# Kernel tuning notes

Hardware: AMD Instinct MI355X
Metric: run time of the kernel (lower is better)

## Reference

```python
import jax, jax.numpy as jnp
import numpy as np

D_MODEL = 768
HEAD_SIZE = 64

def setup_inputs() -> dict:
    key = jax.random.key(0)
    ks = jax.random.split(key, 7)
    B, S = 8, 2048
    x = jax.random.normal(ks[0], (B, S, D_MODEL), dtype=jnp.float32)
    s = 1.0 / np.sqrt(D_MODEL)
    Wq = jax.random.uniform(ks[1], (D_MODEL, HEAD_SIZE), jnp.float32, -s, s)
    bq = jnp.zeros((HEAD_SIZE,), jnp.float32)
    Wk = jax.random.uniform(ks[2], (D_MODEL, HEAD_SIZE), jnp.float32, -s, s)
    bk = jnp.zeros((HEAD_SIZE,), jnp.float32)
    Wv = jax.random.uniform(ks[3], (D_MODEL, HEAD_SIZE), jnp.float32, -s, s)
    bv = jnp.zeros((HEAD_SIZE,), jnp.float32)
    return {"x": x, "Wq": Wq, "bq": bq, "Wk": Wk, "bk": bk, "Wv": Wv, "bv": bv}

def reference(x, Wq, bq, Wk, bk, Wv, bv):
    # Single attention head: softmax(Q K^T / sqrt(head_size)) V
    q = jnp.einsum('bsd,dh->bsh', x, Wq) + bq  # [B,S,H]
    k = jnp.einsum('bsd,dh->bsh', x, Wk) + bk
    v = jnp.einsum('bsd,dh->bsh', x, Wv) + bv
    scale = 1.0 / jnp.sqrt(jnp.array(HEAD_SIZE, dtype=x.dtype))
    scores = jnp.einsum('bqh,bkh->bqk', q, k) * scale  # [B,S,S]
    attn = jax.nn.softmax(scores, axis=-1)
    out = jnp.einsum('bqk,bkh->bqh', attn, v)  # [B,S,H]
    return out
```

## Files before the change

kernel.cpp:

```cpp
#include <hip/hip_runtime.h>
#include <math.h>

#define D_MODEL 768
#define HS 64
#define BATCH 8
#define SEQ 2048
#define SCALE 0.125f
#define KSPLIT 8
#define KCHUNK (SEQ / KSPLIT)

typedef _Float16 half_t;
typedef __attribute__((ext_vector_type(8))) _Float16 half8;
typedef __attribute__((ext_vector_type(4))) float floatx4;

typedef const __attribute__((address_space(1))) void gas_void;
typedef __attribute__((address_space(3))) void las_void;
__device__ __forceinline__ void gl_lds16(const void* g, void* l) {
    __builtin_amdgcn_global_load_lds((gas_void*)g, (las_void*)l, 16, 0, 0);
}
__device__ __forceinline__ void waitcnt_all() {
    __builtin_amdgcn_s_waitcnt(0);
}

__global__ __launch_bounds__(256)
void wconv_kernel(const float* __restrict__ Wq, const float* __restrict__ Wk,
                  const float* __restrict__ Wv, half_t* __restrict__ Wt)
{
    int m = blockIdx.x >> 6;
    int h = blockIdx.x & 63;
    const float* W = (m == 0) ? Wq : ((m == 1) ? Wk : Wv);
    half_t* dst = Wt + (size_t)blockIdx.x * D_MODEL;
    for (int k = threadIdx.x; k < D_MODEL; k += 256)
        dst[k] = (half_t)W[(size_t)k * HS + h];
}

__global__ __launch_bounds__(256)
void proj_kernel(const float* __restrict__ x, const half_t* __restrict__ Wt,
                 const float* __restrict__ bq, const float* __restrict__ bk,
                 const float* __restrict__ bv,
                 half_t* __restrict__ Qh, half_t* __restrict__ Kh,
                 half_t* __restrict__ Vt)
{
    __shared__ __align__(16) half_t xs[2][64 * 64];
    __shared__ __align__(16) half_t wt[2][192 * 64];

    const int tid = threadIdx.x;
    const int w = tid >> 6;
    const int lane = tid & 63;
    const int l15 = lane & 15;
    const int quad = lane >> 4;
    const long row0 = (long)blockIdx.x * 64;

    floatx4 acc[4][3];
#pragma unroll
    for (int i = 0; i < 4; ++i)
#pragma unroll
        for (int j = 0; j < 3; ++j) acc[i][j] = (floatx4){0.f, 0.f, 0.f, 0.f};

    float4 xA[4], xB[4];
    half8  wA[6], wB[6];

    auto loadx = [&](int k0, float4 (&v)[4]) {
#pragma unroll
        for (int i = 0; i < 2; ++i) {
            int idx = i * 256 + tid;
            int r = idx >> 3, sc = idx & 7;
            int cg = sc ^ (r & 7);
            const float* p = x + (row0 + r) * D_MODEL + k0 + cg * 8;
            v[i * 2]     = *(const float4*)p;
            v[i * 2 + 1] = *(const float4*)(p + 4);
        }
    };
    auto loadw = [&](int k0, half8 (&wr)[6]) {
#pragma unroll
        for (int i = 0; i < 6; ++i) {
            int idx = i * 256 + tid;
            int r = idx >> 3, sc = idx & 7;
            int cg = sc ^ (r & 7);
            wr[i] = *(const half8*)(Wt + (size_t)r * D_MODEL + k0 + cg * 8);
        }
    };

    auto step = [&](int it, float4 (&xc)[4], half8 (&wc)[6],
                    float4 (&xn)[4], half8 (&wn)[6], int p) {
#pragma unroll
        for (int i = 0; i < 2; ++i) {
            float4 a = xc[i * 2], b = xc[i * 2 + 1];
            half8 xh = (half8){(half_t)a.x, (half_t)a.y, (half_t)a.z, (half_t)a.w,
                               (half_t)b.x, (half_t)b.y, (half_t)b.z, (half_t)b.w};
            *(half8*)&xs[p][(i * 256 + tid) * 8] = xh;
        }
#pragma unroll
        for (int i = 0; i < 6; ++i)
            *(half8*)&wt[p][(i * 256 + tid) * 8] = wc[i];
        __syncthreads();
        int kn = (it + 1 < 12) ? (it + 1) * 64 : 0;
        loadx(kn, xn);
        loadw(kn, wn);
#pragma unroll
        for (int kst = 0; kst < 2; ++kst) {
            half8 af[4];
#pragma unroll
            for (int mt = 0; mt < 4; ++mt) {
                int r = mt * 16 + l15;
                int slot = (kst * 4 + quad) ^ (r & 7);
                af[mt] = *(const half8*)&xs[p][r * 64 + slot * 8];
            }
#pragma unroll
            for (int nt = 0; nt < 3; ++nt) {
                int r = w * 48 + nt * 16 + l15;
                int slot = (kst * 4 + quad) ^ (r & 7);
                half8 bf = *(const half8*)&wt[p][r * 64 + slot * 8];
#pragma unroll
                for (int mt = 0; mt < 4; ++mt)
                    acc[mt][nt] = __builtin_amdgcn_mfma_f32_16x16x32_f16(
                        af[mt], bf, acc[mt][nt], 0, 0, 0);
            }
        }
    };

    loadx(0, xA);
    loadw(0, wA);
#pragma unroll
    for (int it = 0; it < 12; it += 2) {
        step(it,     xA, wA, xB, wB, 0);
        step(it + 1, xB, wB, xA, wA, 1);
    }

#pragma unroll
    for (int nt = 0; nt < 3; ++nt) {
        int nbase = w * 48 + nt * 16;
        int mm = nbase >> 6;
        int h = (nbase + l15) & 63;
        const float* bias = (mm == 0) ? bq : ((mm == 1) ? bk : bv);
        float bval = bias[h];
#pragma unroll
        for (int mt = 0; mt < 4; ++mt)
#pragma unroll
            for (int r = 0; r < 4; ++r) {
                long R = row0 + mt * 16 + quad * 4 + r;
                half_t hv = (half_t)(acc[mt][nt][r] + bval);
                if (mm == 0)      Qh[R * HS + h] = hv;
                else if (mm == 1) Kh[R * HS + h] = hv;
                else {
                    long bb = R >> 11, s = R & 2047;
                    Vt[(bb * HS + h) * SEQ + s] = hv;
                }
            }
    }
}

__global__ __launch_bounds__(128)
void attn_kernel(const half_t* __restrict__ Qh, const half_t* __restrict__ Kh,
                 const half_t* __restrict__ Vt,
                 half_t* __restrict__ Opart, float* __restrict__ lpart)
{
    __shared__ __align__(16) half_t ks[64 * 64];
    __shared__ __align__(16) half_t vs[64 * 64];
    __shared__ __align__(16) half_t ps[2][16][72];

    const int tid = threadIdx.x;
    const int w = tid >> 6;
    const int lane = tid & 63;
    const int l15 = lane & 15;
    const int quad = lane >> 4;
    const int b = blockIdx.y;
    const int q0 = blockIdx.x * 128 + w * 64;
    const int kh = blockIdx.z;
    const int kk_begin = kh * KCHUNK;

    const half_t* Kb = Kh + (size_t)b * SEQ * HS;
    const half_t* Vb = Vt + (size_t)b * HS * SEQ;

    half8 qf[4][2];
#pragma unroll
    for (int mt = 0; mt < 4; ++mt)
#pragma unroll
        for (int kst = 0; kst < 2; ++kst) {
            half8 q = *(const half8*)(Qh + ((size_t)b * SEQ + q0 + mt * 16 + l15) * HS
                                      + kst * 32 + quad * 8);
#pragma unroll
            for (int j = 0; j < 8; ++j) q[j] = q[j] * (half_t)SCALE;
            qf[mt][kst] = q;
        }

    floatx4 oacc[4][4];
    float lsum[4][4];
#pragma unroll
    for (int mt = 0; mt < 4; ++mt) {
#pragma unroll
        for (int nt = 0; nt < 4; ++nt) oacc[mt][nt] = (floatx4){0.f, 0.f, 0.f, 0.f};
#pragma unroll
        for (int r = 0; r < 4; ++r) lsum[mt][r] = 0.f;
    }

    for (int it = 0; it < KCHUNK / 64; ++it) {
        const int kk0 = kk_begin + it * 64;
        __syncthreads();
#pragma unroll
        for (int i = 0; i < 4; ++i) {
            int idx = i * 128 + tid;
            int r = idx >> 3, sc = idx & 7;
            int cg = sc ^ (r & 7);
            gl_lds16(Kb + (size_t)(kk0 + r) * HS + cg * 8, ks + idx * 8);
            gl_lds16(Vb + (size_t)r * SEQ + kk0 + cg * 8, vs + idx * 8);
        }
        waitcnt_all();
        __syncthreads();

        half8 vf[4][2];
#pragma unroll
        for (int nt = 0; nt < 4; ++nt)
#pragma unroll
            for (int kst = 0; kst < 2; ++kst) {
                int r = nt * 16 + l15;
                int slot = (kst * 4 + quad) ^ (r & 7);
                vf[nt][kst] = *(const half8*)&vs[r * 64 + slot * 8];
            }

#pragma unroll
        for (int h2 = 0; h2 < 2; ++h2) {
            floatx4 sacc[2][4];
#pragma unroll
            for (int mtl = 0; mtl < 2; ++mtl)
#pragma unroll
                for (int nt = 0; nt < 4; ++nt) sacc[mtl][nt] = (floatx4){0.f, 0.f, 0.f, 0.f};
#pragma unroll
            for (int nt = 0; nt < 4; ++nt)
#pragma unroll
                for (int kst = 0; kst < 2; ++kst) {
                    int r = nt * 16 + l15;
                    int slot = (kst * 4 + quad) ^ (r & 7);
                    half8 kf = *(const half8*)&ks[r * 64 + slot * 8];
#pragma unroll
                    for (int mtl = 0; mtl < 2; ++mtl)
                        sacc[mtl][nt] = __builtin_amdgcn_mfma_f32_16x16x32_f16(
                            qf[h2 * 2 + mtl][kst], kf, sacc[mtl][nt], 0, 0, 0);
                }

#pragma unroll
            for (int mtl = 0; mtl < 2; ++mtl) {
                int mt = h2 * 2 + mtl;
#pragma unroll
                for (int nt = 0; nt < 4; ++nt)
#pragma unroll
                    for (int r = 0; r < 4; ++r) {
                        float pv = __expf(sacc[mtl][nt][r]);
                        lsum[mt][r] += pv;
                        ps[w][quad * 4 + r][nt * 16 + l15] = (half_t)pv;
                    }
                half8 pfr[2];
#pragma unroll
                for (int kst = 0; kst < 2; ++kst)
                    pfr[kst] = *(const half8*)&ps[w][l15][kst * 32 + quad * 8];
#pragma unroll
                for (int nt = 0; nt < 4; ++nt)
#pragma unroll
                    for (int kst = 0; kst < 2; ++kst)
                        oacc[mt][nt] = __builtin_amdgcn_mfma_f32_16x16x32_f16(
                            pfr[kst], vf[nt][kst], oacc[mt][nt], 0, 0, 0);
            }
        }
    }

#pragma unroll
    for (int mt = 0; mt < 4; ++mt)
#pragma unroll
        for (int r = 0; r < 4; ++r) {
            float s = lsum[mt][r];
            s += __shfl_xor(s, 1);
            s += __shfl_xor(s, 2);
            s += __shfl_xor(s, 4);
            s += __shfl_xor(s, 8);
            lsum[mt][r] = s;
        }

    size_t obase = ((size_t)kh * BATCH + b) * SEQ * HS;
#pragma unroll
    for (int mt = 0; mt < 4; ++mt)
#pragma unroll
        for (int nt = 0; nt < 4; ++nt)
#pragma unroll
            for (int r = 0; r < 4; ++r) {
                int row = q0 + mt * 16 + quad * 4 + r;
                Opart[obase + (size_t)row * HS + nt * 16 + l15] = (half_t)oacc[mt][nt][r];
            }
    if (l15 == 0) {
#pragma unroll
        for (int mt = 0; mt < 4; ++mt)
#pragma unroll
            for (int r = 0; r < 4; ++r) {
                int row = q0 + mt * 16 + quad * 4 + r;
                lpart[((size_t)kh * BATCH + b) * SEQ + row] = lsum[mt][r];
            }
    }
}

__global__ __launch_bounds__(256)
void combine_kernel(const half_t* __restrict__ Opart, const float* __restrict__ lpart,
                    float* __restrict__ out)
{
    const size_t NT = (size_t)BATCH * SEQ * HS;
    const size_t BS = (size_t)BATCH * SEQ;
    size_t e0 = ((size_t)blockIdx.x * 256 + threadIdx.x) * 8;
    size_t row = e0 / HS;
    float o[8] = {0, 0, 0, 0, 0, 0, 0, 0};
    float l = 0.f;
#pragma unroll
    for (int i = 0; i < KSPLIT; ++i) {
        half8 oi = *(const half8*)(Opart + (size_t)i * NT + e0);
#pragma unroll
        for (int j = 0; j < 8; ++j) o[j] += (float)oi[j];
        l += lpart[(size_t)i * BS + row];
    }
    float inv = 1.f / l;
    float4 a = {o[0] * inv, o[1] * inv, o[2] * inv, o[3] * inv};
    float4 c = {o[4] * inv, o[5] * inv, o[6] * inv, o[7] * inv};
    *(float4*)(out + e0) = a;
    *(float4*)(out + e0 + 4) = c;
}

extern "C" void kernel_launch(void* const* d_in, const int* in_sizes, int n_in,
                              void* d_out, int out_size, void* d_ws, size_t ws_size,
                              hipStream_t stream) {
    const float* x  = (const float*)d_in[0];
    const float* Wq = (const float*)d_in[1];
    const float* bq = (const float*)d_in[2];
    const float* Wk = (const float*)d_in[3];
    const float* bk = (const float*)d_in[4];
    const float* Wv = (const float*)d_in[5];
    const float* bv = (const float*)d_in[6];
    float* out = (float*)d_out;

    const size_t per = (size_t)BATCH * SEQ * HS;
    half_t* Qh = (half_t*)d_ws;
    half_t* Kh = Qh + per;
    half_t* Vt = Kh + per;
    half_t* Wt = Vt + per;
    half_t* Opart = Wt + 3 * HS * D_MODEL;
    float*  lpart = (float*)(Opart + (size_t)KSPLIT * per);

    wconv_kernel<<<dim3(3 * HS), dim3(256), 0, stream>>>(Wq, Wk, Wv, Wt);
    proj_kernel<<<dim3(BATCH * SEQ / 64), dim3(256), 0, stream>>>(
        x, Wt, bq, bk, bv, Qh, Kh, Vt);
    attn_kernel<<<dim3(SEQ / 128, BATCH, KSPLIT), dim3(128), 0, stream>>>(
        Qh, Kh, Vt, Opart, lpart);
    combine_kernel<<<dim3((BATCH * SEQ * HS) / (256 * 8)), dim3(256), 0, stream>>>(
        Opart, lpart, out);
}
```

Before: 140.3 us.

## Double-buffer K/V tiles in attention and halve projection row tile

The attention kernel now keeps two LDS buffers for K and V and issues the global-to-LDS load of the next 64-key tile before computing on the current one, so load latency overlaps with MFMA work. The projection kernel processes 32 rows per block instead of 64, doubling the grid to improve occupancy and load balance. In exchange, attention LDS use grows, and each projection block reloads the full weight tile for half as many rows, which doubles weight traffic per row.

After: 135.5 us. 1.04x faster.

```diff
diff --git a/kernel.cpp b/kernel.cpp
--- a/kernel.cpp
+++ b/kernel.cpp
@@ -8,6 +8,7 @@
 #define SCALE 0.125f
 #define KSPLIT 8
 #define KCHUNK (SEQ / KSPLIT)
+#define PM 32
 
 typedef _Float16 half_t;
 typedef __attribute__((ext_vector_type(8))) _Float16 half8;
@@ -41,7 +42,7 @@
                  half_t* __restrict__ Qh, half_t* __restrict__ Kh,
                  half_t* __restrict__ Vt)
 {
-    __shared__ __align__(16) half_t xs[2][64 * 64];
+    __shared__ __align__(16) half_t xs[2][PM * 64];
     __shared__ __align__(16) half_t wt[2][192 * 64];
 
     const int tid = threadIdx.x;
@@ -49,27 +50,23 @@
     const int lane = tid & 63;
     const int l15 = lane & 15;
     const int quad = lane >> 4;
-    const long row0 = (long)blockIdx.x * 64;
-
-    floatx4 acc[4][3];
-#pragma unroll
-    for (int i = 0; i < 4; ++i)
+    const long row0 = (long)blockIdx.x * PM;
+
+    floatx4 acc[2][3];
+#pragma unroll
+    for (int i = 0; i < 2; ++i)
 #pragma unroll
         for (int j = 0; j < 3; ++j) acc[i][j] = (floatx4){0.f, 0.f, 0.f, 0.f};
 
-    float4 xA[4], xB[4];
+    float4 xA[2], xB[2];
     half8  wA[6], wB[6];
 
-    auto loadx = [&](int k0, float4 (&v)[4]) {
-#pragma unroll
-        for (int i = 0; i < 2; ++i) {
-            int idx = i * 256 + tid;
-            int r = idx >> 3, sc = idx & 7;
-            int cg = sc ^ (r & 7);
-            const float* p = x + (row0 + r) * D_MODEL + k0 + cg * 8;
-            v[i * 2]     = *(const float4*)p;
-            v[i * 2 + 1] = *(const float4*)(p + 4);
-        }
+    auto loadx = [&](int k0, float4 (&v)[2]) {
+        int r = tid >> 3, sc = tid & 7;
+        int cg = sc ^ (r & 7);
+        const float* p = x + (row0 + r) * D_MODEL + k0 + cg * 8;
+        v[0] = *(const float4*)p;
+        v[1] = *(const float4*)(p + 4);
     };
     auto loadw = [&](int k0, half8 (&wr)[6]) {
 #pragma unroll
@@ -81,14 +78,13 @@
         }
     };
 
-    auto step = [&](int it, float4 (&xc)[4], half8 (&wc)[6],
-                    float4 (&xn)[4], half8 (&wn)[6], int p) {
-#pragma unroll
-        for (int i = 0; i < 2; ++i) {
-            float4 a = xc[i * 2], b = xc[i * 2 + 1];
+    auto step = [&](int it, float4 (&xc)[2], half8 (&wc)[6],
+                    float4 (&xn)[2], half8 (&wn)[6], int p) {
+        {
+            float4 a = xc[0], b = xc[1];
             half8 xh = (half8){(half_t)a.x, (half_t)a.y, (half_t)a.z, (half_t)a.w,
                                (half_t)b.x, (half_t)b.y, (half_t)b.z, (half_t)b.w};
-            *(half8*)&xs[p][(i * 256 + tid) * 8] = xh;
+            *(half8*)&xs[p][tid * 8] = xh;
         }
 #pragma unroll
         for (int i = 0; i < 6; ++i)
@@ -99,9 +95,9 @@
         loadw(kn, wn);
 #pragma unroll
         for (int kst = 0; kst < 2; ++kst) {
-            half8 af[4];
-#pragma unroll
-            for (int mt = 0; mt < 4; ++mt) {
+            half8 af[2];
+#pragma unroll
+            for (int mt = 0; mt < 2; ++mt) {
                 int r = mt * 16 + l15;
                 int slot = (kst * 4 + quad) ^ (r & 7);
                 af[mt] = *(const half8*)&xs[p][r * 64 + slot * 8];
@@ -112,7 +108,7 @@
                 int slot = (kst * 4 + quad) ^ (r & 7);
                 half8 bf = *(const half8*)&wt[p][r * 64 + slot * 8];
 #pragma unroll
-                for (int mt = 0; mt < 4; ++mt)
+                for (int mt = 0; mt < 2; ++mt)
                     acc[mt][nt] = __builtin_amdgcn_mfma_f32_16x16x32_f16(
                         af[mt], bf, acc[mt][nt], 0, 0, 0);
             }
@@ -135,7 +131,7 @@
         const float* bias = (mm == 0) ? bq : ((mm == 1) ? bk : bv);
         float bval = bias[h];
 #pragma unroll
-        for (int mt = 0; mt < 4; ++mt)
+        for (int mt = 0; mt < 2; ++mt)
 #pragma unroll
             for (int r = 0; r < 4; ++r) {
                 long R = row0 + mt * 16 + quad * 4 + r;
@@ -155,8 +151,8 @@
                  const half_t* __restrict__ Vt,
                  half_t* __restrict__ Opart, float* __restrict__ lpart)
 {
-    __shared__ __align__(16) half_t ks[64 * 64];
-    __shared__ __align__(16) half_t vs[64 * 64];
+    __shared__ __align__(16) half_t ks[2][64 * 64];
+    __shared__ __align__(16) half_t vs[2][64 * 64];
     __shared__ __align__(16) half_t ps[2][16][72];
 
     const int tid = threadIdx.x;
@@ -194,19 +190,25 @@
         for (int r = 0; r < 4; ++r) lsum[mt][r] = 0.f;
     }
 
-    for (int it = 0; it < KCHUNK / 64; ++it) {
-        const int kk0 = kk_begin + it * 64;
-        __syncthreads();
+    auto stage = [&](int p, int kk0) {
 #pragma unroll
         for (int i = 0; i < 4; ++i) {
             int idx = i * 128 + tid;
             int r = idx >> 3, sc = idx & 7;
             int cg = sc ^ (r & 7);
-            gl_lds16(Kb + (size_t)(kk0 + r) * HS + cg * 8, ks + idx * 8);
-            gl_lds16(Vb + (size_t)r * SEQ + kk0 + cg * 8, vs + idx * 8);
-        }
+            gl_lds16(Kb + (size_t)(kk0 + r) * HS + cg * 8, &ks[p][idx * 8]);
+            gl_lds16(Vb + (size_t)r * SEQ + kk0 + cg * 8, &vs[p][idx * 8]);
+        }
+    };
+
+    stage(0, kk_begin);
+
+    for (int it = 0; it < KCHUNK / 64; ++it) {
+        const int cur = it & 1;
         waitcnt_all();
         __syncthreads();
+        if (it + 1 < KCHUNK / 64)
+            stage(cur ^ 1, kk_begin + (it + 1) * 64);
 
         half8 vf[4][2];
 #pragma unroll
@@ -215,7 +217,7 @@
             for (int kst = 0; kst < 2; ++kst) {
                 int r = nt * 16 + l15;
                 int slot = (kst * 4 + quad) ^ (r & 7);
-                vf[nt][kst] = *(const half8*)&vs[r * 64 + slot * 8];
+                vf[nt][kst] = *(const half8*)&vs[cur][r * 64 + slot * 8];
             }
 
 #pragma unroll
@@ -231,7 +233,7 @@
                 for (int kst = 0; kst < 2; ++kst) {
                     int r = nt * 16 + l15;
                     int slot = (kst * 4 + quad) ^ (r & 7);
-                    half8 kf = *(const half8*)&ks[r * 64 + slot * 8];
+                    half8 kf = *(const half8*)&ks[cur][r * 64 + slot * 8];
 #pragma unroll
                     for (int mtl = 0; mtl < 2; ++mtl)
                         sacc[mtl][nt] = __builtin_amdgcn_mfma_f32_16x16x32_f16(
@@ -341,7 +343,7 @@
     float*  lpart = (float*)(Opart + (size_t)KSPLIT * per);
 
     wconv_kernel<<<dim3(3 * HS), dim3(256), 0, stream>>>(Wq, Wk, Wv, Wt);
-    proj_kernel<<<dim3(BATCH * SEQ / 64), dim3(256), 0, stream>>>(
+    proj_kernel<<<dim3(BATCH * SEQ / PM), dim3(256), 0, stream>>>(
         x, Wt, bq, bk, bv, Qh, Kh, Vt);
     attn_kernel<<<dim3(SEQ / 128, BATCH, KSPLIT), dim3(128), 0, stream>>>(
         Qh, Kh, Vt, Opart, lpart);
```
